# Performance work log

Hardware: AMD Instinct MI355X
Metric: run time of the kernel (lower is better)

The kernel has to match this reference:

```python
import jax, jax.numpy as jnp
import numpy as np

N_NODES = 100000
N_EDGES = 1600000
D_IN = 64
D_OUT = 64
CLAMP = -10000.0  # scatter_'max' post-clamp threshold from the source


def setup_inputs() -> dict:
    key = jax.random.key(0)
    k1, k2, k3, k4, k5 = jax.random.split(key, 5)
    n_feat = jax.random.normal(k1, (N_NODES, D_IN), dtype=jnp.float32)
    src = jax.random.randint(k2, (N_EDGES,), 0, N_NODES, dtype=jnp.int64)
    dst = jax.random.randint(k3, (N_EDGES,), 0, N_NODES, dtype=jnp.int64)
    W = jax.random.normal(k4, (2 * D_IN, D_OUT), dtype=jnp.float32) / np.sqrt(2 * D_IN)
    b = jax.random.normal(k5, (D_OUT,), dtype=jnp.float32) * 0.01
    return {"n_feat": n_feat, "src": src, "dst": dst, "W": W, "b": b}


def reference(n_feat, src, dst, W, b):
    # gather endpoint features and form relative messages: [E, d]
    diff = n_feat[src] - n_feat[dst]
    # scatter-max aggregate onto destination nodes: [N, d]
    agg = jax.ops.segment_max(diff, dst, num_segments=n_feat.shape[0])
    # torch_scatter fills empty slots with lowest value; source clamps out<-10000 to 0
    agg = jnp.where(agg < CLAMP, 0.0, agg)
    # concat original + aggregated, then MLP = Linear + ReLU: [N, 2d] @ [2d, out]
    h = jnp.concatenate([n_feat, agg], axis=1)
    return jax.nn.relu(h @ W + b)
```

## Files before the change

kernel.cpp:

```cpp
#include <hip/hip_runtime.h>
#include <hip/hip_bf16.h>

#define D 64
#define CLAMP_V -10000.0f
#define SBSHIFT 9
#define SBN 512
#define MAXSB 256
#define HCHUNK 4096
#define SCHUNK 4096
#define NPW 8

typedef __bf16 bf16x4 __attribute__((ext_vector_type(4)));
typedef __bf16 bf16x8 __attribute__((ext_vector_type(8)));
typedef float floatx4 __attribute__((ext_vector_type(4)));
typedef unsigned short u16x2 __attribute__((ext_vector_type(2)));
typedef short s16x2 __attribute__((ext_vector_type(2)));

__device__ __forceinline__ unsigned pkmax(unsigned a, unsigned b) {
    u16x2 r = __builtin_elementwise_max(__builtin_bit_cast(u16x2, a),
                                        __builtin_bit_cast(u16x2, b));
    return __builtin_bit_cast(unsigned, r);
}
__device__ __forceinline__ unsigned pk_ord_encode(unsigned g) {
    s16x2 t = __builtin_bit_cast(s16x2, g) >> 15;
    unsigned m = __builtin_bit_cast(unsigned, t) & 0x7FFF7FFFu;
    return g ^ (m | 0x80008000u);
}
__device__ __forceinline__ unsigned pk_ord_decode(unsigned e) {
    s16x2 t = __builtin_bit_cast(s16x2, e) >> 15;
    unsigned m = (~__builtin_bit_cast(unsigned, t)) & 0x7FFF7FFFu;
    return e ^ (m | 0x80008000u);
}

__global__ __launch_bounds__(256) void prep_kernel(
        const float* __restrict__ nf, __bf16* __restrict__ nf16, int n4,
        const int* __restrict__ dst, unsigned* __restrict__ ghist,
        int nE, int nbSB,
        const float* __restrict__ W, __bf16* __restrict__ wfrag,
        int histBlocks, int wBlock) {
    __shared__ unsigned h[MAXSB];
    int blk = blockIdx.x, t = threadIdx.x;
    int i = blk * 256 + t;
    if (i < n4) {
        float4 v = ((const float4*)nf)[i];
        bf16x4 o = { (__bf16)v.x, (__bf16)v.y, (__bf16)v.z, (__bf16)v.w };
        ((bf16x4*)nf16)[i] = o;
    }
    if (blk < histBlocks) {
        if (t < MAXSB) h[t] = 0;
        __syncthreads();
        int e0 = blk * HCHUNK;
        int ec = nE - e0; if (ec > HCHUNK) ec = HCHUNK;
        for (int k = t; k < ec; k += 256) atomicAdd(&h[dst[e0 + k] >> SBSHIFT], 1u);
        __syncthreads();
        if (t < (unsigned)nbSB && h[t]) atomicAdd(&ghist[t], h[t]);
    }
    if (blk == wBlock) {
        for (int idx = t; idx < 2 * D * D; idx += 256) {
            int k = idx >> 6, n = idx & 63;
            int ks = k >> 5, r = k & 31, quad = r >> 3, j = r & 7;
            int c = n >> 4, l16 = n & 15;
            int fidx = (((ks * 4 + c) * 64) + quad * 16 + l16) * 8 + j;
            wfrag[fidx] = (__bf16)W[idx];
        }
    }
}

__global__ __launch_bounds__(256) void scan_sb(
        const unsigned* __restrict__ ghist, unsigned* __restrict__ base,
        unsigned* __restrict__ cursor, int nbSB) {
    __shared__ unsigned ts[256];
    int t = threadIdx.x;
    unsigned v = (t < nbSB) ? ghist[t] : 0u;
    ts[t] = v; __syncthreads();
    for (int off = 1; off < 256; off <<= 1) {
        unsigned x = (t >= off) ? ts[t - off] : 0u;
        __syncthreads();
        ts[t] += x;
        __syncthreads();
    }
    if (t < nbSB) {
        unsigned ex = ts[t] - v;
        base[t] = ex; cursor[t] = ex;
        if (t == nbSB - 1) base[nbSB] = ts[t];
    }
}

__global__ __launch_bounds__(256) void sb_scatter(
        const int* __restrict__ src, const int* __restrict__ dst,
        unsigned* __restrict__ cursor, unsigned* __restrict__ packed,
        int nE, int nbSB) {
    __shared__ unsigned cop[MAXSB];
    __shared__ unsigned short lb16[MAXSB];
    __shared__ unsigned gbase[MAXSB];
    __shared__ unsigned payload[SCHUNK];
    __shared__ unsigned char sbid[SCHUNK];
    __shared__ unsigned ts[256];
    int t = threadIdx.x;
    int e0 = blockIdx.x * SCHUNK;
    int ec = nE - e0; if (ec > SCHUNK) ec = SCHUNK;

    if (t < MAXSB) cop[t] = 0;
    __syncthreads();
    for (int i = t; i < ec; i += 256)
        atomicAdd(&cop[dst[e0 + i] >> SBSHIFT], 1u);
    __syncthreads();
    unsigned c = (t < nbSB) ? (cop[t] & 0xFFFFu) : 0u;
    ts[t] = c; __syncthreads();
    for (int o = 1; o < 256; o <<= 1) {
        unsigned x = (t >= o) ? ts[t - o] : 0u;
        __syncthreads();
        ts[t] += x;
        __syncthreads();
    }
    if (t < nbSB) {
        lb16[t] = (unsigned short)(ts[t] - c);
        if (c) gbase[t] = atomicAdd(&cursor[t], c);
    }
    __syncthreads();
    for (int i = t; i < ec; i += 256) {
        int e = e0 + i;
        int d = dst[e];
        int b = d >> SBSHIFT;
        unsigned p = atomicAdd(&cop[b], 0x10000u) >> 16;
        unsigned pos = (unsigned)lb16[b] + p;
        payload[pos] = ((unsigned)(d & (SBN - 1)) << 17) | (unsigned)src[e];
        sbid[pos] = (unsigned char)b;
    }
    __syncthreads();
    for (int i = t; i < ec; i += 256) {
        unsigned b = sbid[i];
        packed[gbase[b] + ((unsigned)i - (unsigned)lb16[b])] = payload[i];
    }
}

__global__ __launch_bounds__(256) void sb_sort(
        const unsigned* __restrict__ packed1, const unsigned* __restrict__ base,
        unsigned* __restrict__ packed2, unsigned* __restrict__ nodestart,
        int nN) {
    __shared__ unsigned cnt[SBN];
    __shared__ unsigned ts[256];
    int sb = blockIdx.x, t = threadIdx.x;
    unsigned beg = base[sb], end = base[sb + 1];
    cnt[2 * t] = 0; cnt[2 * t + 1] = 0;
    __syncthreads();
    for (unsigned i = beg + t; i < end; i += 256)
        atomicAdd(&cnt[packed1[i] >> 17], 1u);
    __syncthreads();
    unsigned a = cnt[2 * t], b = cnt[2 * t + 1], s = a + b;
    ts[t] = s; __syncthreads();
    for (int o = 1; o < 256; o <<= 1) {
        unsigned x = (t >= o) ? ts[t - o] : 0u;
        __syncthreads();
        ts[t] += x;
        __syncthreads();
    }
    unsigned ex = ts[t] - s;
    cnt[2 * t] = ex; cnt[2 * t + 1] = ex + a;
    int n0 = sb * SBN;
    if (n0 + 2 * t     <= nN) nodestart[n0 + 2 * t]     = beg + ex;
    if (n0 + 2 * t + 1 <= nN) nodestart[n0 + 2 * t + 1] = beg + ex + a;
    __syncthreads();
    for (unsigned i = beg + t; i < end; i += 256) {
        unsigned e = packed1[i];
        unsigned p = atomicAdd(&cnt[e >> 17], 1u);
        packed2[beg + p] = e & 0x1FFFFu;
    }
}

__global__ __launch_bounds__(256) void seg_direct(
        const unsigned* __restrict__ nfu,
        const unsigned* __restrict__ packed2,
        const unsigned* __restrict__ nodestart,
        unsigned* __restrict__ agg16u,
        int nN) {
    int t = threadIdx.x;
    int wv = t >> 6, ln = t & 63;
    int half = ln >> 5, dln = ln & 31;
    int n0 = blockIdx.x * (4 * NPW) + wv * NPW;
    #pragma unroll 1
    for (int k = 0; k < NPW; ++k) {
        int n = n0 + k;
        if (n >= nN) break;
        unsigned rb = nodestart[n], re = nodestart[n + 1];
        unsigned m0 = 0, m1 = 0, m2 = 0, m3 = 0;
        for (unsigned c = rb; c < re; c += 64) {
            unsigned idx = c + (unsigned)ln;
            unsigned pe = (idx < re) ? packed2[idx] : 0u;
            int lim = (int)(re - c); if (lim > 64) lim = 64;
            int j = 0;
            for (; j + 8 <= lim; j += 8) {
                unsigned sa = __shfl(pe, j + half, 64);
                unsigned sb = __shfl(pe, j + 2 + half, 64);
                unsigned sc = __shfl(pe, j + 4 + half, 64);
                unsigned sd = __shfl(pe, j + 6 + half, 64);
                unsigned g0 = nfu[(size_t)sa * 32 + dln];
                unsigned g1 = nfu[(size_t)sb * 32 + dln];
                unsigned g2 = nfu[(size_t)sc * 32 + dln];
                unsigned g3 = nfu[(size_t)sd * 32 + dln];
                m0 = pkmax(m0, pk_ord_encode(g0));
                m1 = pkmax(m1, pk_ord_encode(g1));
                m2 = pkmax(m2, pk_ord_encode(g2));
                m3 = pkmax(m3, pk_ord_encode(g3));
            }
            for (; j + 4 <= lim; j += 4) {
                unsigned sa = __shfl(pe, j + half, 64);
                unsigned sb = __shfl(pe, j + 2 + half, 64);
                unsigned g0 = nfu[(size_t)sa * 32 + dln];
                unsigned g1 = nfu[(size_t)sb * 32 + dln];
                m0 = pkmax(m0, pk_ord_encode(g0));
                m1 = pkmax(m1, pk_ord_encode(g1));
            }
            for (; j < lim; j += 2) {
                int jj = j + half;
                if (jj >= lim) jj = lim - 1;
                unsigned g = nfu[(size_t)__shfl(pe, jj, 64) * 32 + dln];
                m0 = pkmax(m0, pk_ord_encode(g));
            }
        }
        unsigned m = pkmax(pkmax(m0, m1), pkmax(m2, m3));
        m = pkmax(m, __shfl_xor(m, 32, 64));
        if (ln < 32) {
            unsigned raw = pk_ord_decode(m);
            unsigned xr  = nfu[(size_t)n * 32 + dln];
            float v0 = __uint_as_float(raw << 16);
            float v1 = __uint_as_float(raw & 0xFFFF0000u);
            float x0 = __uint_as_float(xr << 16);
            float x1 = __uint_as_float(xr & 0xFFFF0000u);
            float r0 = v0 - x0; r0 = (r0 >= CLAMP_V) ? r0 : 0.0f;
            float r1 = v1 - x1; r1 = (r1 >= CLAMP_V) ? r1 : 0.0f;
            __bf16 b0 = (__bf16)r0, b1 = (__bf16)r1;
            unsigned o = ((unsigned)__builtin_bit_cast(unsigned short, b1) << 16)
                       |  (unsigned)__builtin_bit_cast(unsigned short, b0);
            agg16u[(size_t)n * 32 + dln] = o;
        }
    }
}

__global__ __launch_bounds__(256) void node_mlp_mfma(
        const __bf16* __restrict__ nf16,
        const __bf16* __restrict__ agg16,
        float* __restrict__ out,
        const __bf16* __restrict__ wfrag,
        const float* __restrict__ bias,
        int nTiles, int nN) {
    int lane = threadIdx.x & 63;
    int quad = lane >> 4;
    int l16  = lane & 15;
    int waveGlobal = blockIdx.x * 4 + (threadIdx.x >> 6);
    int nWaves = gridDim.x * 4;

    bf16x8 bfrag[4][4];
    #pragma unroll
    for (int c = 0; c < 4; ++c)
        #pragma unroll
        for (int ks = 0; ks < 4; ++ks)
            bfrag[c][ks] = *(const bf16x8*)(wfrag + ((size_t)((ks * 4 + c) * 64 + lane)) * 8);
    float bv[4];
    #pragma unroll
    for (int c = 0; c < 4; ++c) bv[c] = bias[c * 16 + l16];

    for (int t = waveGlobal; t < nTiles; t += nWaves) {
        int n0 = t * 16;
        int rowA = n0 + l16;
        if (rowA >= nN) rowA = nN - 1;
        const __bf16* nfr = nf16  + (size_t)rowA * D;
        const __bf16* agr = agg16 + (size_t)rowA * D;

        floatx4 acc[4] = {{0,0,0,0},{0,0,0,0},{0,0,0,0},{0,0,0,0}};
        #pragma unroll
        for (int ks = 0; ks < 4; ++ks) {
            const __bf16* p = (ks < 2) ? (nfr + ks * 32 + quad * 8)
                                       : (agr + (ks - 2) * 32 + quad * 8);
            bf16x8 a = *(const bf16x8*)p;
            #pragma unroll
            for (int c = 0; c < 4; ++c)
                acc[c] = __builtin_amdgcn_mfma_f32_16x16x32_bf16(
                             a, bfrag[c][ks], acc[c], 0, 0, 0);
        }
        #pragma unroll
        for (int r = 0; r < 4; ++r) {
            int row = n0 + quad * 4 + r;
            if (row < nN) {
                #pragma unroll
                for (int c = 0; c < 4; ++c) {
                    float vv = acc[c][r] + bv[c];
                    out[(size_t)row * D + c * 16 + l16] = fmaxf(vv, 0.0f);
                }
            }
        }
    }
}

extern "C" void kernel_launch(void* const* d_in, const int* in_sizes, int n_in,
                              void* d_out, int out_size, void* d_ws, size_t ws_size,
                              hipStream_t stream) {
    const float* nf  = (const float*)d_in[0];
    const int*   src = (const int*)d_in[1];
    const int*   dst = (const int*)d_in[2];
    const float* W   = (const float*)d_in[3];
    const float* b   = (const float*)d_in[4];
    float* out = (float*)d_out;

    int nN = in_sizes[0] / D;
    int nE = in_sizes[1];
    int nbSB = (nN + SBN - 1) / SBN;

    char* wsb = (char*)d_ws;
    size_t nfB  = (((size_t)nN * D * 2) + 255) & ~(size_t)255;
    size_t pkB  = (((size_t)nE * 4)     + 255) & ~(size_t)255;
    __bf16*   nf16   = (__bf16*)wsb;
    __bf16*   agg16  = (__bf16*)(wsb + nfB);
    unsigned* packed1 = (unsigned*)(wsb + 2 * nfB);
    unsigned* ghist  = (unsigned*)(wsb + 2 * nfB + pkB);
    unsigned* base   = (unsigned*)(wsb + 2 * nfB + pkB + 4 * MAXSB);
    unsigned* cursor = (unsigned*)(wsb + 2 * nfB + pkB + 4 * MAXSB + 4 * (MAXSB + 2));
    __bf16*   wfrag  = (__bf16*)(wsb + 2 * nfB + pkB + 4 * MAXSB + 8 * (MAXSB + 2));
    unsigned* nodestart = (unsigned*)(wsb + 2 * nfB + pkB + 4 * MAXSB
                                      + 8 * (MAXSB + 2) + 32768);
    unsigned* packed2 = (unsigned*)d_out;

    hipMemsetAsync(ghist, 0, (size_t)nbSB * 4, stream);

    int n4 = nN * D / 4;
    int convBlocks = (n4 + 255) / 256;
    int histBlocks = (nE + HCHUNK - 1) / HCHUNK;
    int gridPrep = convBlocks > histBlocks ? convBlocks : histBlocks;
    prep_kernel<<<gridPrep, 256, 0, stream>>>(nf, nf16, n4, dst, ghist, nE, nbSB,
                                              W, wfrag, histBlocks, gridPrep - 1);

    scan_sb<<<1, 256, 0, stream>>>(ghist, base, cursor, nbSB);

    int nbS = (nE + SCHUNK - 1) / SCHUNK;
    sb_scatter<<<nbS, 256, 0, stream>>>(src, dst, cursor, packed1, nE, nbSB);

    sb_sort<<<nbSB, 256, 0, stream>>>(packed1, base, packed2, nodestart, nN);

    int segBlocks = (nN + 4 * NPW - 1) / (4 * NPW);
    seg_direct<<<segBlocks, 256, 0, stream>>>(
        (const unsigned*)nf16, packed2, nodestart, (unsigned*)agg16, nN);

    int nTiles = (nN + 15) / 16;
    node_mlp_mfma<<<768, 256, 0, stream>>>(nf16, agg16, out, wfrag, b, nTiles, nN);
}
```

Before: 200.7 us.

## Fold superblock scan into consumers, split sort into quarters, deepen gather unroll

Removes the single-block scan kernel: each scatter and sort block recomputes the prefix sum of the superblock histogram redundantly, and the cursor becomes a zero-initialised offset added to the recomputed base. The sort kernel now launches four blocks per superblock, each counting the whole superblock per quarter and scattering only its own quarter, so there are more blocks in flight and the tail shrinks. The scatter chunk size is halved to launch more blocks, and the segment gather loop is unrolled to 16 edges so more loads are in flight. In exchange, the scan and the counting pass are repeated in every block, and there is more redundant reading of packed1 in the sort.

```diff
diff --git a/kernel.cpp b/kernel.cpp
--- a/kernel.cpp
+++ b/kernel.cpp
@@ -7,7 +7,7 @@
 #define SBN 512
 #define MAXSB 256
 #define HCHUNK 4096
-#define SCHUNK 4096
+#define SCHUNK 2048
 #define NPW 8
 
 typedef __bf16 bf16x4 __attribute__((ext_vector_type(4)));
@@ -66,30 +66,10 @@
     }
 }
 
-__global__ __launch_bounds__(256) void scan_sb(
-        const unsigned* __restrict__ ghist, unsigned* __restrict__ base,
-        unsigned* __restrict__ cursor, int nbSB) {
-    __shared__ unsigned ts[256];
-    int t = threadIdx.x;
-    unsigned v = (t < nbSB) ? ghist[t] : 0u;
-    ts[t] = v; __syncthreads();
-    for (int off = 1; off < 256; off <<= 1) {
-        unsigned x = (t >= off) ? ts[t - off] : 0u;
-        __syncthreads();
-        ts[t] += x;
-        __syncthreads();
-    }
-    if (t < nbSB) {
-        unsigned ex = ts[t] - v;
-        base[t] = ex; cursor[t] = ex;
-        if (t == nbSB - 1) base[nbSB] = ts[t];
-    }
-}
-
 __global__ __launch_bounds__(256) void sb_scatter(
         const int* __restrict__ src, const int* __restrict__ dst,
-        unsigned* __restrict__ cursor, unsigned* __restrict__ packed,
-        int nE, int nbSB) {
+        const unsigned* __restrict__ ghist, unsigned* __restrict__ cursor0,
+        unsigned* __restrict__ packed, int nE, int nbSB) {
     __shared__ unsigned cop[MAXSB];
     __shared__ unsigned short lb16[MAXSB];
     __shared__ unsigned gbase[MAXSB];
@@ -100,6 +80,16 @@
     int e0 = blockIdx.x * SCHUNK;
     int ec = nE - e0; if (ec > SCHUNK) ec = SCHUNK;
 
+    unsigned g = (t < nbSB) ? ghist[t] : 0u;
+    ts[t] = g; __syncthreads();
+    for (int o = 1; o < 256; o <<= 1) {
+        unsigned x = (t >= o) ? ts[t - o] : 0u;
+        __syncthreads();
+        ts[t] += x;
+        __syncthreads();
+    }
+    unsigned myBase = ts[t] - g;
+
     if (t < MAXSB) cop[t] = 0;
     __syncthreads();
     for (int i = t; i < ec; i += 256)
@@ -115,7 +105,7 @@
     }
     if (t < nbSB) {
         lb16[t] = (unsigned short)(ts[t] - c);
-        if (c) gbase[t] = atomicAdd(&cursor[t], c);
+        if (c) gbase[t] = myBase + atomicAdd(&cursor0[t], c);
     }
     __syncthreads();
     for (int i = t; i < ec; i += 256) {
@@ -135,19 +125,44 @@
 }
 
 __global__ __launch_bounds__(256) void sb_sort(
-        const unsigned* __restrict__ packed1, const unsigned* __restrict__ base,
+        const unsigned* __restrict__ packed1, const unsigned* __restrict__ ghist,
         unsigned* __restrict__ packed2, unsigned* __restrict__ nodestart,
-        int nN) {
-    __shared__ unsigned cnt[SBN];
+        int nbSB, int nN) {
+    __shared__ unsigned cnt[4][SBN];
+    __shared__ unsigned cur[SBN];
     __shared__ unsigned ts[256];
-    int sb = blockIdx.x, t = threadIdx.x;
-    unsigned beg = base[sb], end = base[sb + 1];
-    cnt[2 * t] = 0; cnt[2 * t + 1] = 0;
-    __syncthreads();
-    for (unsigned i = beg + t; i < end; i += 256)
-        atomicAdd(&cnt[packed1[i] >> 17], 1u);
-    __syncthreads();
-    unsigned a = cnt[2 * t], b = cnt[2 * t + 1], s = a + b;
+    int blk = blockIdx.x;
+    int sb = blk >> 2, q = blk & 3;
+    int t = threadIdx.x;
+
+    unsigned g = (t < nbSB) ? ghist[t] : 0u;
+    ts[t] = g; __syncthreads();
+    for (int o = 1; o < 256; o <<= 1) {
+        unsigned x = (t >= o) ? ts[t - o] : 0u;
+        __syncthreads();
+        ts[t] += x;
+        __syncthreads();
+    }
+    __shared__ unsigned sBegEnd[2];
+    if (t == sb) { sBegEnd[0] = ts[t] - g; sBegEnd[1] = ts[t]; }
+    __syncthreads();
+    unsigned beg = sBegEnd[0], end = sBegEnd[1];
+    unsigned len = end - beg;
+    unsigned qlen = (len + 3) >> 2;
+
+    for (int i = t; i < 4 * SBN; i += 256) ((unsigned*)cnt)[i] = 0;
+    __syncthreads();
+    for (unsigned i = beg + t; i < end; i += 256) {
+        unsigned e = packed1[i];
+        unsigned r = i - beg;
+        unsigned qq = (r >= qlen) + (r >= 2 * qlen) + (r >= 3 * qlen);
+        atomicAdd(&cnt[qq][e >> 17], 1u);
+    }
+    __syncthreads();
+    unsigned a0 = cnt[0][2 * t] + cnt[1][2 * t] + cnt[2][2 * t] + cnt[3][2 * t];
+    unsigned a1 = cnt[0][2 * t + 1] + cnt[1][2 * t + 1]
+                + cnt[2][2 * t + 1] + cnt[3][2 * t + 1];
+    unsigned s = a0 + a1;
     ts[t] = s; __syncthreads();
     for (int o = 1; o < 256; o <<= 1) {
         unsigned x = (t >= o) ? ts[t - o] : 0u;
@@ -156,15 +171,24 @@
         __syncthreads();
     }
     unsigned ex = ts[t] - s;
-    cnt[2 * t] = ex; cnt[2 * t + 1] = ex + a;
     int n0 = sb * SBN;
-    if (n0 + 2 * t     <= nN) nodestart[n0 + 2 * t]     = beg + ex;
-    if (n0 + 2 * t + 1 <= nN) nodestart[n0 + 2 * t + 1] = beg + ex + a;
-    __syncthreads();
-    for (unsigned i = beg + t; i < end; i += 256) {
+    if (q == 0) {
+        if (n0 + 2 * t     <= nN) nodestart[n0 + 2 * t]     = beg + ex;
+        if (n0 + 2 * t + 1 <= nN) nodestart[n0 + 2 * t + 1] = beg + ex + a0;
+    }
+    unsigned p0 = 0, p1 = 0;
+    for (int p = 0; p < 4; ++p) {
+        if (p < q) { p0 += cnt[p][2 * t]; p1 += cnt[p][2 * t + 1]; }
+    }
+    cur[2 * t]     = beg + ex + p0;
+    cur[2 * t + 1] = beg + ex + a0 + p1;
+    __syncthreads();
+    unsigned qb = beg + q * qlen;
+    unsigned qe = qb + qlen; if (qe > end) qe = end;
+    for (unsigned i = qb + t; i < qe; i += 256) {
         unsigned e = packed1[i];
-        unsigned p = atomicAdd(&cnt[e >> 17], 1u);
-        packed2[beg + p] = e & 0x1FFFFu;
+        unsigned p = atomicAdd(&cur[e >> 17], 1u);
+        packed2[p] = e & 0x1FFFFu;
     }
 }
 
@@ -189,25 +213,51 @@
             unsigned pe = (idx < re) ? packed2[idx] : 0u;
             int lim = (int)(re - c); if (lim > 64) lim = 64;
             int j = 0;
-            for (; j + 8 <= lim; j += 8) {
-                unsigned sa = __shfl(pe, j + half, 64);
-                unsigned sb = __shfl(pe, j + 2 + half, 64);
-                unsigned sc = __shfl(pe, j + 4 + half, 64);
-                unsigned sd = __shfl(pe, j + 6 + half, 64);
-                unsigned g0 = nfu[(size_t)sa * 32 + dln];
-                unsigned g1 = nfu[(size_t)sb * 32 + dln];
-                unsigned g2 = nfu[(size_t)sc * 32 + dln];
-                unsigned g3 = nfu[(size_t)sd * 32 + dln];
+            for (; j + 16 <= lim; j += 16) {
+                unsigned s0 = __shfl(pe, j + half, 64);
+                unsigned s1 = __shfl(pe, j + 2 + half, 64);
+                unsigned s2 = __shfl(pe, j + 4 + half, 64);
+                unsigned s3 = __shfl(pe, j + 6 + half, 64);
+                unsigned s4 = __shfl(pe, j + 8 + half, 64);
+                unsigned s5 = __shfl(pe, j + 10 + half, 64);
+                unsigned s6 = __shfl(pe, j + 12 + half, 64);
+                unsigned s7 = __shfl(pe, j + 14 + half, 64);
+                unsigned g0 = nfu[(size_t)s0 * 32 + dln];
+                unsigned g1 = nfu[(size_t)s1 * 32 + dln];
+                unsigned g2 = nfu[(size_t)s2 * 32 + dln];
+                unsigned g3 = nfu[(size_t)s3 * 32 + dln];
+                unsigned g4 = nfu[(size_t)s4 * 32 + dln];
+                unsigned g5 = nfu[(size_t)s5 * 32 + dln];
+                unsigned g6 = nfu[(size_t)s6 * 32 + dln];
+                unsigned g7 = nfu[(size_t)s7 * 32 + dln];
                 m0 = pkmax(m0, pk_ord_encode(g0));
                 m1 = pkmax(m1, pk_ord_encode(g1));
                 m2 = pkmax(m2, pk_ord_encode(g2));
                 m3 = pkmax(m3, pk_ord_encode(g3));
+                m0 = pkmax(m0, pk_ord_encode(g4));
+                m1 = pkmax(m1, pk_ord_encode(g5));
+                m2 = pkmax(m2, pk_ord_encode(g6));
+                m3 = pkmax(m3, pk_ord_encode(g7));
+            }
+            for (; j + 8 <= lim; j += 8) {
+                unsigned s0 = __shfl(pe, j + half, 64);
+                unsigned s1 = __shfl(pe, j + 2 + half, 64);
+                unsigned s2 = __shfl(pe, j + 4 + half, 64);
+                unsigned s3 = __shfl(pe, j + 6 + half, 64);
+                unsigned g0 = nfu[(size_t)s0 * 32 + dln];
+                unsigned g1 = nfu[(size_t)s1 * 32 + dln];
+                unsigned g2 = nfu[(size_t)s2 * 32 + dln];
+                unsigned g3 = nfu[(size_t)s3 * 32 + dln];
+                m0 = pkmax(m0, pk_ord_encode(g0));
+                m1 = pkmax(m1, pk_ord_encode(g1));
+                m2 = pkmax(m2, pk_ord_encode(g2));
+                m3 = pkmax(m3, pk_ord_encode(g3));
             }
             for (; j + 4 <= lim; j += 4) {
-                unsigned sa = __shfl(pe, j + half, 64);
-                unsigned sb = __shfl(pe, j + 2 + half, 64);
-                unsigned g0 = nfu[(size_t)sa * 32 + dln];
-                unsigned g1 = nfu[(size_t)sb * 32 + dln];
+                unsigned s0 = __shfl(pe, j + half, 64);
+                unsigned s1 = __shfl(pe, j + 2 + half, 64);
+                unsigned g0 = nfu[(size_t)s0 * 32 + dln];
+                unsigned g1 = nfu[(size_t)s1 * 32 + dln];
                 m0 = pkmax(m0, pk_ord_encode(g0));
                 m1 = pkmax(m1, pk_ord_encode(g1));
             }
@@ -309,18 +359,16 @@
     char* wsb = (char*)d_ws;
     size_t nfB  = (((size_t)nN * D * 2) + 255) & ~(size_t)255;
     size_t pkB  = (((size_t)nE * 4)     + 255) & ~(size_t)255;
-    __bf16*   nf16   = (__bf16*)wsb;
-    __bf16*   agg16  = (__bf16*)(wsb + nfB);
+    __bf16*   nf16    = (__bf16*)wsb;
+    __bf16*   agg16   = (__bf16*)(wsb + nfB);
     unsigned* packed1 = (unsigned*)(wsb + 2 * nfB);
-    unsigned* ghist  = (unsigned*)(wsb + 2 * nfB + pkB);
-    unsigned* base   = (unsigned*)(wsb + 2 * nfB + pkB + 4 * MAXSB);
-    unsigned* cursor = (unsigned*)(wsb + 2 * nfB + pkB + 4 * MAXSB + 4 * (MAXSB + 2));
-    __bf16*   wfrag  = (__bf16*)(wsb + 2 * nfB + pkB + 4 * MAXSB + 8 * (MAXSB + 2));
-    unsigned* nodestart = (unsigned*)(wsb + 2 * nfB + pkB + 4 * MAXSB
-                                      + 8 * (MAXSB + 2) + 32768);
+    unsigned* ghist   = (unsigned*)(wsb + 2 * nfB + pkB);
+    unsigned* cursor0 = (unsigned*)(wsb + 2 * nfB + pkB + 4 * MAXSB);
+    __bf16*   wfrag   = (__bf16*)(wsb + 2 * nfB + pkB + 8 * MAXSB);
+    unsigned* nodestart = (unsigned*)(wsb + 2 * nfB + pkB + 8 * MAXSB + 32768);
     unsigned* packed2 = (unsigned*)d_out;
 
-    hipMemsetAsync(ghist, 0, (size_t)nbSB * 4, stream);
+    hipMemsetAsync(ghist, 0, 8 * MAXSB, stream);
 
     int n4 = nN * D / 4;
     int convBlocks = (n4 + 255) / 256;
@@ -329,12 +377,11 @@
     prep_kernel<<<gridPrep, 256, 0, stream>>>(nf, nf16, n4, dst, ghist, nE, nbSB,
                                               W, wfrag, histBlocks, gridPrep - 1);
 
-    scan_sb<<<1, 256, 0, stream>>>(ghist, base, cursor, nbSB);
-
     int nbS = (nE + SCHUNK - 1) / SCHUNK;
-    sb_scatter<<<nbS, 256, 0, stream>>>(src, dst, cursor, packed1, nE, nbSB);
-
-    sb_sort<<<nbSB, 256, 0, stream>>>(packed1, base, packed2, nodestart, nN);
+    sb_scatter<<<nbS, 256, 0, stream>>>(src, dst, ghist, cursor0, packed1, nE, nbSB);
+
+    sb_sort<<<nbSB * 4, 256, 0, stream>>>(packed1, ghist, packed2, nodestart,
+                                          nbSB, nN);
 
     int segBlocks = (nN + 4 * NPW - 1) / (4 * NPW);
     seg_direct<<<segBlocks, 256, 0, stream>>>(
```

Result: slower. 204.9 us (+2.1%).

## Fuse preprocessing, bucketing, sort and segment-max into one cooperative kernel

Applied to the files above, without the earlier changes.

Replaces five separate launches (prep/histogram, scan, superblock scatter, per-superblock sort, segment max) with a single cooperative kernel that uses grid-wide syncs between phases. The histogram now counts per node with global atomics, so node offsets come straight from a per-superblock reduce and scan, and the sort pass no longer recounts. This removes launch gaps and the tiny single-block scan kernel. In exchange it adds several grid.sync barriers, heavy global atomic contention on per-node counters, and a fixed 1024-block grid that must be co-resident.

```diff
diff --git a/kernel.cpp b/kernel.cpp
--- a/kernel.cpp
+++ b/kernel.cpp
@@ -1,14 +1,17 @@
 #include <hip/hip_runtime.h>
 #include <hip/hip_bf16.h>
+#include <hip/hip_cooperative_groups.h>
+
+namespace cg = cooperative_groups;
 
 #define D 64
 #define CLAMP_V -10000.0f
 #define SBSHIFT 9
 #define SBN 512
 #define MAXSB 256
-#define HCHUNK 4096
-#define SCHUNK 4096
+#define SCHUNK 2048
 #define NPW 8
+#define GRIDC 1024
 
 typedef __bf16 bf16x4 __attribute__((ext_vector_type(4)));
 typedef __bf16 bf16x8 __attribute__((ext_vector_type(8)));
@@ -32,30 +35,45 @@
     return e ^ (m | 0x80008000u);
 }
 
-__global__ __launch_bounds__(256) void prep_kernel(
-        const float* __restrict__ nf, __bf16* __restrict__ nf16, int n4,
-        const int* __restrict__ dst, unsigned* __restrict__ ghist,
-        int nE, int nbSB,
+union SharedU {
+    unsigned ts[256];
+    struct {
+        unsigned cop[MAXSB];
+        unsigned short lb16[MAXSB];
+        unsigned gbase[MAXSB];
+        unsigned payload[SCHUNK];
+        unsigned char sbid[SCHUNK];
+        unsigned ts2[256];
+    } p3;
+    unsigned cur[SBN];
+};
+
+__global__ __launch_bounds__(256, 4) void fused_kernel(
+        const float* __restrict__ nf, __bf16* __restrict__ nf16,
+        const int* __restrict__ src, const int* __restrict__ dst,
         const float* __restrict__ W, __bf16* __restrict__ wfrag,
-        int histBlocks, int wBlock) {
-    __shared__ unsigned h[MAXSB];
-    int blk = blockIdx.x, t = threadIdx.x;
-    int i = blk * 256 + t;
-    if (i < n4) {
+        unsigned* __restrict__ nodecnt,
+        unsigned* __restrict__ nodestart,
+        unsigned* __restrict__ sbTotal,
+        unsigned* __restrict__ cursor0,
+        unsigned* __restrict__ packed1,
+        unsigned* __restrict__ packed2,
+        unsigned* __restrict__ agg16u,
+        int n4, int nE, int nbSB, int nN, int nChunks, int nGroups) {
+    cg::grid_group grid = cg::this_grid();
+    __shared__ SharedU sh;
+    int t = threadIdx.x;
+    int blk = blockIdx.x;
+    int nBlk = gridDim.x;
+
+    for (int i = blk * 256 + t; i < n4; i += nBlk * 256) {
         float4 v = ((const float4*)nf)[i];
         bf16x4 o = { (__bf16)v.x, (__bf16)v.y, (__bf16)v.z, (__bf16)v.w };
         ((bf16x4*)nf16)[i] = o;
     }
-    if (blk < histBlocks) {
-        if (t < MAXSB) h[t] = 0;
-        __syncthreads();
-        int e0 = blk * HCHUNK;
-        int ec = nE - e0; if (ec > HCHUNK) ec = HCHUNK;
-        for (int k = t; k < ec; k += 256) atomicAdd(&h[dst[e0 + k] >> SBSHIFT], 1u);
-        __syncthreads();
-        if (t < (unsigned)nbSB && h[t]) atomicAdd(&ghist[t], h[t]);
-    }
-    if (blk == wBlock) {
+    for (int e = blk * 256 + t; e < nE; e += nBlk * 256)
+        atomicAdd(&nodecnt[dst[e]], 1u);
+    if (blk == nBlk - 1) {
         for (int idx = t; idx < 2 * D * D; idx += 256) {
             int k = idx >> 6, n = idx & 63;
             int ks = k >> 5, r = k & 31, quad = r >> 3, j = r & 7;
@@ -64,175 +82,175 @@
             wfrag[fidx] = (__bf16)W[idx];
         }
     }
-}
-
-__global__ __launch_bounds__(256) void scan_sb(
-        const unsigned* __restrict__ ghist, unsigned* __restrict__ base,
-        unsigned* __restrict__ cursor, int nbSB) {
-    __shared__ unsigned ts[256];
-    int t = threadIdx.x;
-    unsigned v = (t < nbSB) ? ghist[t] : 0u;
-    ts[t] = v; __syncthreads();
-    for (int off = 1; off < 256; off <<= 1) {
-        unsigned x = (t >= off) ? ts[t - off] : 0u;
-        __syncthreads();
-        ts[t] += x;
-        __syncthreads();
-    }
-    if (t < nbSB) {
-        unsigned ex = ts[t] - v;
-        base[t] = ex; cursor[t] = ex;
-        if (t == nbSB - 1) base[nbSB] = ts[t];
-    }
-}
-
-__global__ __launch_bounds__(256) void sb_scatter(
-        const int* __restrict__ src, const int* __restrict__ dst,
-        unsigned* __restrict__ cursor, unsigned* __restrict__ packed,
-        int nE, int nbSB) {
-    __shared__ unsigned cop[MAXSB];
-    __shared__ unsigned short lb16[MAXSB];
-    __shared__ unsigned gbase[MAXSB];
-    __shared__ unsigned payload[SCHUNK];
-    __shared__ unsigned char sbid[SCHUNK];
-    __shared__ unsigned ts[256];
-    int t = threadIdx.x;
-    int e0 = blockIdx.x * SCHUNK;
-    int ec = nE - e0; if (ec > SCHUNK) ec = SCHUNK;
-
-    if (t < MAXSB) cop[t] = 0;
-    __syncthreads();
-    for (int i = t; i < ec; i += 256)
-        atomicAdd(&cop[dst[e0 + i] >> SBSHIFT], 1u);
-    __syncthreads();
-    unsigned c = (t < nbSB) ? (cop[t] & 0xFFFFu) : 0u;
-    ts[t] = c; __syncthreads();
-    for (int o = 1; o < 256; o <<= 1) {
-        unsigned x = (t >= o) ? ts[t - o] : 0u;
-        __syncthreads();
-        ts[t] += x;
-        __syncthreads();
-    }
-    if (t < nbSB) {
-        lb16[t] = (unsigned short)(ts[t] - c);
-        if (c) gbase[t] = atomicAdd(&cursor[t], c);
-    }
-    __syncthreads();
-    for (int i = t; i < ec; i += 256) {
-        int e = e0 + i;
-        int d = dst[e];
-        int b = d >> SBSHIFT;
-        unsigned p = atomicAdd(&cop[b], 0x10000u) >> 16;
-        unsigned pos = (unsigned)lb16[b] + p;
-        payload[pos] = ((unsigned)(d & (SBN - 1)) << 17) | (unsigned)src[e];
-        sbid[pos] = (unsigned char)b;
-    }
-    __syncthreads();
-    for (int i = t; i < ec; i += 256) {
-        unsigned b = sbid[i];
-        packed[gbase[b] + ((unsigned)i - (unsigned)lb16[b])] = payload[i];
-    }
-}
-
-__global__ __launch_bounds__(256) void sb_sort(
-        const unsigned* __restrict__ packed1, const unsigned* __restrict__ base,
-        unsigned* __restrict__ packed2, unsigned* __restrict__ nodestart,
-        int nN) {
-    __shared__ unsigned cnt[SBN];
-    __shared__ unsigned ts[256];
-    int sb = blockIdx.x, t = threadIdx.x;
-    unsigned beg = base[sb], end = base[sb + 1];
-    cnt[2 * t] = 0; cnt[2 * t + 1] = 0;
-    __syncthreads();
-    for (unsigned i = beg + t; i < end; i += 256)
-        atomicAdd(&cnt[packed1[i] >> 17], 1u);
-    __syncthreads();
-    unsigned a = cnt[2 * t], b = cnt[2 * t + 1], s = a + b;
-    ts[t] = s; __syncthreads();
-    for (int o = 1; o < 256; o <<= 1) {
-        unsigned x = (t >= o) ? ts[t - o] : 0u;
-        __syncthreads();
-        ts[t] += x;
-        __syncthreads();
-    }
-    unsigned ex = ts[t] - s;
-    cnt[2 * t] = ex; cnt[2 * t + 1] = ex + a;
-    int n0 = sb * SBN;
-    if (n0 + 2 * t     <= nN) nodestart[n0 + 2 * t]     = beg + ex;
-    if (n0 + 2 * t + 1 <= nN) nodestart[n0 + 2 * t + 1] = beg + ex + a;
-    __syncthreads();
-    for (unsigned i = beg + t; i < end; i += 256) {
-        unsigned e = packed1[i];
-        unsigned p = atomicAdd(&cnt[e >> 17], 1u);
-        packed2[beg + p] = e & 0x1FFFFu;
-    }
-}
-
-__global__ __launch_bounds__(256) void seg_direct(
-        const unsigned* __restrict__ nfu,
-        const unsigned* __restrict__ packed2,
-        const unsigned* __restrict__ nodestart,
-        unsigned* __restrict__ agg16u,
-        int nN) {
-    int t = threadIdx.x;
-    int wv = t >> 6, ln = t & 63;
-    int half = ln >> 5, dln = ln & 31;
-    int n0 = blockIdx.x * (4 * NPW) + wv * NPW;
-    #pragma unroll 1
-    for (int k = 0; k < NPW; ++k) {
-        int n = n0 + k;
-        if (n >= nN) break;
-        unsigned rb = nodestart[n], re = nodestart[n + 1];
-        unsigned m0 = 0, m1 = 0, m2 = 0, m3 = 0;
-        for (unsigned c = rb; c < re; c += 64) {
-            unsigned idx = c + (unsigned)ln;
-            unsigned pe = (idx < re) ? packed2[idx] : 0u;
-            int lim = (int)(re - c); if (lim > 64) lim = 64;
-            int j = 0;
-            for (; j + 8 <= lim; j += 8) {
-                unsigned sa = __shfl(pe, j + half, 64);
-                unsigned sb = __shfl(pe, j + 2 + half, 64);
-                unsigned sc = __shfl(pe, j + 4 + half, 64);
-                unsigned sd = __shfl(pe, j + 6 + half, 64);
-                unsigned g0 = nfu[(size_t)sa * 32 + dln];
-                unsigned g1 = nfu[(size_t)sb * 32 + dln];
-                unsigned g2 = nfu[(size_t)sc * 32 + dln];
-                unsigned g3 = nfu[(size_t)sd * 32 + dln];
-                m0 = pkmax(m0, pk_ord_encode(g0));
-                m1 = pkmax(m1, pk_ord_encode(g1));
-                m2 = pkmax(m2, pk_ord_encode(g2));
-                m3 = pkmax(m3, pk_ord_encode(g3));
-            }
-            for (; j + 4 <= lim; j += 4) {
-                unsigned sa = __shfl(pe, j + half, 64);
-                unsigned sb = __shfl(pe, j + 2 + half, 64);
-                unsigned g0 = nfu[(size_t)sa * 32 + dln];
-                unsigned g1 = nfu[(size_t)sb * 32 + dln];
-                m0 = pkmax(m0, pk_ord_encode(g0));
-                m1 = pkmax(m1, pk_ord_encode(g1));
-            }
-            for (; j < lim; j += 2) {
-                int jj = j + half;
-                if (jj >= lim) jj = lim - 1;
-                unsigned g = nfu[(size_t)__shfl(pe, jj, 64) * 32 + dln];
-                m0 = pkmax(m0, pk_ord_encode(g));
-            }
-        }
-        unsigned m = pkmax(pkmax(m0, m1), pkmax(m2, m3));
-        m = pkmax(m, __shfl_xor(m, 32, 64));
-        if (ln < 32) {
-            unsigned raw = pk_ord_decode(m);
-            unsigned xr  = nfu[(size_t)n * 32 + dln];
-            float v0 = __uint_as_float(raw << 16);
-            float v1 = __uint_as_float(raw & 0xFFFF0000u);
-            float x0 = __uint_as_float(xr << 16);
-            float x1 = __uint_as_float(xr & 0xFFFF0000u);
-            float r0 = v0 - x0; r0 = (r0 >= CLAMP_V) ? r0 : 0.0f;
-            float r1 = v1 - x1; r1 = (r1 >= CLAMP_V) ? r1 : 0.0f;
-            __bf16 b0 = (__bf16)r0, b1 = (__bf16)r1;
-            unsigned o = ((unsigned)__builtin_bit_cast(unsigned short, b1) << 16)
-                       |  (unsigned)__builtin_bit_cast(unsigned short, b0);
-            agg16u[(size_t)n * 32 + dln] = o;
+    grid.sync();
+
+    if (blk < nbSB) {
+        unsigned a = nodecnt[blk * SBN + 2 * t] + nodecnt[blk * SBN + 2 * t + 1];
+        sh.ts[t] = a; __syncthreads();
+        for (int o = 128; o > 0; o >>= 1) {
+            if (t < o) sh.ts[t] += sh.ts[t + o];
+            __syncthreads();
+        }
+        if (t == 0) sbTotal[blk] = sh.ts[0];
+    }
+    grid.sync();
+
+    if (blk < nbSB) {
+        unsigned part = (t < blk) ? sbTotal[t] : 0u;
+        sh.ts[t] = part; __syncthreads();
+        for (int o = 128; o > 0; o >>= 1) {
+            if (t < o) sh.ts[t] += sh.ts[t + o];
+            __syncthreads();
+        }
+        unsigned sbBase = sh.ts[0];
+        __syncthreads();
+        unsigned a0 = nodecnt[blk * SBN + 2 * t];
+        unsigned a1 = nodecnt[blk * SBN + 2 * t + 1];
+        unsigned s = a0 + a1;
+        sh.ts[t] = s; __syncthreads();
+        for (int o = 1; o < 256; o <<= 1) {
+            unsigned x = (t >= o) ? sh.ts[t - o] : 0u;
+            __syncthreads();
+            sh.ts[t] += x;
+            __syncthreads();
+        }
+        unsigned ex = sh.ts[t] - s;
+        nodestart[blk * SBN + 2 * t]     = sbBase + ex;
+        nodestart[blk * SBN + 2 * t + 1] = sbBase + ex + a0;
+        __syncthreads();
+    }
+
+    {
+        unsigned g = (t < nbSB) ? sbTotal[t] : 0u;
+        sh.p3.ts2[t] = g; __syncthreads();
+        for (int o = 1; o < 256; o <<= 1) {
+            unsigned x = (t >= o) ? sh.p3.ts2[t - o] : 0u;
+            __syncthreads();
+            sh.p3.ts2[t] += x;
+            __syncthreads();
+        }
+        unsigned myBase = sh.p3.ts2[t] - g;
+        __syncthreads();
+
+        for (int ch = blk; ch < nChunks; ch += nBlk) {
+            int e0 = ch * SCHUNK;
+            int ec = nE - e0; if (ec > SCHUNK) ec = SCHUNK;
+            if (t < MAXSB) sh.p3.cop[t] = 0;
+            __syncthreads();
+            for (int i = t; i < ec; i += 256)
+                atomicAdd(&sh.p3.cop[dst[e0 + i] >> SBSHIFT], 1u);
+            __syncthreads();
+            unsigned c = (t < nbSB) ? (sh.p3.cop[t] & 0xFFFFu) : 0u;
+            sh.p3.ts2[t] = c; __syncthreads();
+            for (int o = 1; o < 256; o <<= 1) {
+                unsigned x = (t >= o) ? sh.p3.ts2[t - o] : 0u;
+                __syncthreads();
+                sh.p3.ts2[t] += x;
+                __syncthreads();
+            }
+            if (t < nbSB) {
+                sh.p3.lb16[t] = (unsigned short)(sh.p3.ts2[t] - c);
+                if (c) sh.p3.gbase[t] = myBase + atomicAdd(&cursor0[t], c);
+            }
+            __syncthreads();
+            for (int i = t; i < ec; i += 256) {
+                int e = e0 + i;
+                int d = dst[e];
+                int b = d >> SBSHIFT;
+                unsigned p = atomicAdd(&sh.p3.cop[b], 0x10000u) >> 16;
+                unsigned pos = (unsigned)sh.p3.lb16[b] + p;
+                sh.p3.payload[pos] = ((unsigned)(d & (SBN - 1)) << 17) | (unsigned)src[e];
+                sh.p3.sbid[pos] = (unsigned char)b;
+            }
+            __syncthreads();
+            for (int i = t; i < ec; i += 256) {
+                unsigned b = sh.p3.sbid[i];
+                packed1[sh.p3.gbase[b] + ((unsigned)i - (unsigned)sh.p3.lb16[b])]
+                    = sh.p3.payload[i];
+            }
+            __syncthreads();
+        }
+    }
+    grid.sync();
+
+    for (int sb = blk; sb < nbSB; sb += nBlk) {
+        unsigned beg = nodestart[sb * SBN];
+        unsigned cnt = sbTotal[sb];
+        sh.cur[2 * t]     = nodestart[sb * SBN + 2 * t];
+        sh.cur[2 * t + 1] = nodestart[sb * SBN + 2 * t + 1];
+        __syncthreads();
+        for (unsigned i = beg + t; i < beg + cnt; i += 256) {
+            unsigned e = packed1[i];
+            unsigned p = atomicAdd(&sh.cur[e >> 17], 1u);
+            packed2[p] = e & 0x1FFFFu;
+        }
+        __syncthreads();
+    }
+    grid.sync();
+
+    {
+        const unsigned* nfu = (const unsigned*)nf16;
+        int wv = t >> 6, ln = t & 63;
+        int half = ln >> 5, dln = ln & 31;
+        for (int grp = blk; grp < nGroups; grp += nBlk) {
+            int n0 = grp * (4 * NPW) + wv * NPW;
+            #pragma unroll 1
+            for (int k = 0; k < NPW; ++k) {
+                int n = n0 + k;
+                if (n >= nN) break;
+                unsigned rb = nodestart[n], re = nodestart[n + 1];
+                unsigned m0 = 0, m1 = 0, m2 = 0, m3 = 0;
+                for (unsigned c = rb; c < re; c += 64) {
+                    unsigned idx = c + (unsigned)ln;
+                    unsigned pe = (idx < re) ? packed2[idx] : 0u;
+                    int lim = (int)(re - c); if (lim > 64) lim = 64;
+                    int j = 0;
+                    for (; j + 8 <= lim; j += 8) {
+                        unsigned sa = __shfl(pe, j + half, 64);
+                        unsigned sb = __shfl(pe, j + 2 + half, 64);
+                        unsigned sc = __shfl(pe, j + 4 + half, 64);
+                        unsigned sd = __shfl(pe, j + 6 + half, 64);
+                        unsigned g0 = nfu[(size_t)sa * 32 + dln];
+                        unsigned g1 = nfu[(size_t)sb * 32 + dln];
+                        unsigned g2 = nfu[(size_t)sc * 32 + dln];
+                        unsigned g3 = nfu[(size_t)sd * 32 + dln];
+                        m0 = pkmax(m0, pk_ord_encode(g0));
+                        m1 = pkmax(m1, pk_ord_encode(g1));
+                        m2 = pkmax(m2, pk_ord_encode(g2));
+                        m3 = pkmax(m3, pk_ord_encode(g3));
+                    }
+                    for (; j + 4 <= lim; j += 4) {
+                        unsigned sa = __shfl(pe, j + half, 64);
+                        unsigned sb = __shfl(pe, j + 2 + half, 64);
+                        unsigned g0 = nfu[(size_t)sa * 32 + dln];
+                        unsigned g1 = nfu[(size_t)sb * 32 + dln];
+                        m0 = pkmax(m0, pk_ord_encode(g0));
+                        m1 = pkmax(m1, pk_ord_encode(g1));
+                    }
+                    for (; j < lim; j += 2) {
+                        int jj = j + half;
+                        if (jj >= lim) jj = lim - 1;
+                        unsigned g = nfu[(size_t)__shfl(pe, jj, 64) * 32 + dln];
+                        m0 = pkmax(m0, pk_ord_encode(g));
+                    }
+                }
+                unsigned m = pkmax(pkmax(m0, m1), pkmax(m2, m3));
+                m = pkmax(m, __shfl_xor(m, 32, 64));
+                if (ln < 32) {
+                    unsigned raw = pk_ord_decode(m);
+                    unsigned xr  = nfu[(size_t)n * 32 + dln];
+                    float v0 = __uint_as_float(raw << 16);
+                    float v1 = __uint_as_float(raw & 0xFFFF0000u);
+                    float x0 = __uint_as_float(xr << 16);
+                    float x1 = __uint_as_float(xr & 0xFFFF0000u);
+                    float r0 = v0 - x0; r0 = (r0 >= CLAMP_V) ? r0 : 0.0f;
+                    float r1 = v1 - x1; r1 = (r1 >= CLAMP_V) ? r1 : 0.0f;
+                    __bf16 b0 = (__bf16)r0, b1 = (__bf16)r1;
+                    unsigned o = ((unsigned)__builtin_bit_cast(unsigned short, b1) << 16)
+                               |  (unsigned)__builtin_bit_cast(unsigned short, b0);
+                    agg16u[(size_t)n * 32 + dln] = o;
+                }
+            }
         }
     }
 }
@@ -309,36 +327,33 @@
     char* wsb = (char*)d_ws;
     size_t nfB  = (((size_t)nN * D * 2) + 255) & ~(size_t)255;
     size_t pkB  = (((size_t)nE * 4)     + 255) & ~(size_t)255;
-    __bf16*   nf16   = (__bf16*)wsb;
-    __bf16*   agg16  = (__bf16*)(wsb + nfB);
-    unsigned* packed1 = (unsigned*)(wsb + 2 * nfB);
-    unsigned* ghist  = (unsigned*)(wsb + 2 * nfB + pkB);
-    unsigned* base   = (unsigned*)(wsb + 2 * nfB + pkB + 4 * MAXSB);
-    unsigned* cursor = (unsigned*)(wsb + 2 * nfB + pkB + 4 * MAXSB + 4 * (MAXSB + 2));
-    __bf16*   wfrag  = (__bf16*)(wsb + 2 * nfB + pkB + 4 * MAXSB + 8 * (MAXSB + 2));
-    unsigned* nodestart = (unsigned*)(wsb + 2 * nfB + pkB + 4 * MAXSB
-                                      + 8 * (MAXSB + 2) + 32768);
+    size_t ncB  = (((size_t)nbSB * SBN * 4) + 255) & ~(size_t)255;
+    __bf16*   nf16      = (__bf16*)wsb;
+    __bf16*   agg16     = (__bf16*)(wsb + nfB);
+    unsigned* packed1   = (unsigned*)(wsb + 2 * nfB);
+    unsigned* nodecnt   = (unsigned*)(wsb + 2 * nfB + pkB);
+    unsigned* cursor0   = (unsigned*)(wsb + 2 * nfB + pkB + ncB);
+    unsigned* nodestart = (unsigned*)(wsb + 2 * nfB + pkB + ncB + 4 * MAXSB);
+    unsigned* sbTotal   = (unsigned*)(wsb + 2 * nfB + pkB + 2 * ncB + 4 * MAXSB + 256);
+    __bf16*   wfrag     = (__bf16*)(wsb + 2 * nfB + pkB + 2 * ncB + 8 * MAXSB + 512);
     unsigned* packed2 = (unsigned*)d_out;
 
-    hipMemsetAsync(ghist, 0, (size_t)nbSB * 4, stream);
+    hipMemsetAsync(nodecnt, 0, ncB + 4 * MAXSB, stream);
 
     int n4 = nN * D / 4;
-    int convBlocks = (n4 + 255) / 256;
-    int histBlocks = (nE + HCHUNK - 1) / HCHUNK;
-    int gridPrep = convBlocks > histBlocks ? convBlocks : histBlocks;
-    prep_kernel<<<gridPrep, 256, 0, stream>>>(nf, nf16, n4, dst, ghist, nE, nbSB,
-                                              W, wfrag, histBlocks, gridPrep - 1);
-
-    scan_sb<<<1, 256, 0, stream>>>(ghist, base, cursor, nbSB);
-
-    int nbS = (nE + SCHUNK - 1) / SCHUNK;
-    sb_scatter<<<nbS, 256, 0, stream>>>(src, dst, cursor, packed1, nE, nbSB);
-
-    sb_sort<<<nbSB, 256, 0, stream>>>(packed1, base, packed2, nodestart, nN);
-
-    int segBlocks = (nN + 4 * NPW - 1) / (4 * NPW);
-    seg_direct<<<segBlocks, 256, 0, stream>>>(
-        (const unsigned*)nf16, packed2, nodestart, (unsigned*)agg16, nN);
+    int nChunks = (nE + SCHUNK - 1) / SCHUNK;
+    int nGroups = (nN + 4 * NPW - 1) / (4 * NPW);
+
+    __bf16* nf16p = nf16;
+    void* args[] = {
+        (void*)&nf, (void*)&nf16p, (void*)&src, (void*)&dst, (void*)&W,
+        (void*)&wfrag, (void*)&nodecnt, (void*)&nodestart, (void*)&sbTotal,
+        (void*)&cursor0, (void*)&packed1, (void*)&packed2, (void*)&agg16,
+        (void*)&n4, (void*)&nE, (void*)&nbSB, (void*)&nN,
+        (void*)&nChunks, (void*)&nGroups
+    };
+    hipLaunchCooperativeKernel((void*)fused_kernel, dim3(GRIDC), dim3(256),
+                               args, 0, stream);
 
     int nTiles = (nN + 15) / 16;
     node_mlp_mfma<<<768, 256, 0, stream>>>(nf16, agg16, out, wfrag, b, nTiles, nN);
```

After: 709.2 us. 253% more time.
